# Kernel optimization log

Measured on AMD Instinct MI355X. Metric: run time of the kernel, lower is better.

The kernel has to match this reference:

```python
import jax, jax.numpy as jnp
import numpy as np

N = 50000      # nodes (src = dst at both layers)
E = 800000     # edges per layer
T = 8          # time steps
C_IN = 16      # input channels
HID = 16       # conv1 out channels (hardcoded in SAGENet)
C_OUT = 32     # final out channels


def setup_inputs() -> dict:
    key = jax.random.key(0)
    ks = jax.random.split(key, 10)
    X = jax.random.normal(ks[0], (T, N, C_IN), dtype=jnp.float32)
    edge_index0 = jax.random.randint(ks[1], (2, E), 0, N, dtype=jnp.int32)
    edge_weight0 = jax.random.uniform(ks[2], (E,), dtype=jnp.float32)
    edge_index1 = jax.random.randint(ks[3], (2, E), 0, N, dtype=jnp.int32)
    edge_weight1 = jax.random.uniform(ks[4], (E,), dtype=jnp.float32)
    res_n_id0 = jnp.arange(N, dtype=jnp.int32)
    res_n_id1 = jnp.arange(N, dtype=jnp.int32)
    W1 = jax.random.normal(ks[5], (2 * C_IN, HID), dtype=jnp.float32) * 0.1
    b1 = jax.random.normal(ks[6], (HID,), dtype=jnp.float32) * 0.1
    W2 = jax.random.normal(ks[7], (2 * HID, C_OUT), dtype=jnp.float32) * 0.1
    b2 = jax.random.normal(ks[8], (C_OUT,), dtype=jnp.float32) * 0.1
    return {"X": X, "edge_index0": edge_index0, "edge_weight0": edge_weight0,
            "edge_index1": edge_index1, "edge_weight1": edge_weight1,
            "res_n_id0": res_n_id0, "res_n_id1": res_n_id1,
            "W1": W1, "b1": b1, "W2": W2, "b2": b2}


def sage_conv(x, edge_index, edge_weight, res_n_id, num_dst, W, b):
    # x: [N_src, T, C]; message = edge_weight * x[src]; mean-aggregate to dst;
    # concat residual x[res_n_id] then linear (old PyG SAGEConv, concat=True).
    src, dst = edge_index[0], edge_index[1]
    msg = x[src] * edge_weight[:, None, None]                      # [E, T, C]
    summed = jax.ops.segment_sum(msg, dst, num_segments=num_dst)   # [Nd, T, C]
    cnt = jax.ops.segment_sum(jnp.ones_like(edge_weight), dst, num_segments=num_dst)
    aggr = summed / jnp.maximum(cnt, 1.0)[:, None, None]
    h = jnp.concatenate([x[res_n_id], aggr], axis=-1)              # [Nd, T, 2C]
    return jnp.einsum('ntc,cd->ntd', h, W) + b


def reference(X, edge_index0, edge_weight0, edge_index1, edge_weight1,
              res_n_id0, res_n_id1, W1, b1, W2, b2):
    x = jnp.transpose(X, (1, 0, 2))                                # [N, T, C]
    x = jax.nn.leaky_relu(sage_conv(x, edge_index0, edge_weight0, res_n_id0, N, W1, b1), 0.01)
    x = jax.nn.leaky_relu(sage_conv(x, edge_index1, edge_weight1, res_n_id1, N, W2, b2), 0.01)
    return jnp.transpose(x, (1, 0, 2))                             # [T, N, C_out]
```

## Files before the change

### kernel.cpp

```cpp
#include <hip/hip_runtime.h>
#include <hip/hip_bf16.h>
#include <stdint.h>

static constexpr int Nn   = 50000;
static constexpr int Ee   = 800000;
static constexpr int Tt   = 8;
static constexpr int CIN  = 16;
static constexpr int HID  = 16;
static constexpr int COUT = 32;
static constexpr int TC   = Tt * CIN;
static constexpr int ROWD = TC / 2;

static constexpr int NB  = (2 * Nn + 255) / 256;
static constexpr int CAP = 16;
static constexpr int GSTR = 32;

static constexpr int BINB = 768;
static constexpr int EPB  = (2 * Ee + BINB - 1) / BINB;
static constexpr int TRB  = 1536;

typedef __attribute__((ext_vector_type(8))) short short8;
typedef __attribute__((ext_vector_type(4))) float f32x4;
union FU { uint4 u4; short8 s8; };

__device__ inline unsigned short f2bf(float x) {
    __hip_bfloat16 h = __float2bfloat16(x);
    unsigned short u; __builtin_memcpy(&u, &h, 2); return u;
}
__device__ inline uint32_t bfpack(float a, float b) {
    return (uint32_t)f2bf(a) | ((uint32_t)f2bf(b) << 16);
}
__device__ inline void redg(float2& a) {
    a.x += __shfl_xor(a.x, 16); a.y += __shfl_xor(a.y, 16);
    a.x += __shfl_xor(a.x, 32); a.y += __shfl_xor(a.y, 32);
}

__device__ inline float dot2bf(float acc, uint32_t w2, uint32_t x2) {
    asm("v_dot2_f32_bf16 %0, %1, %2, %0" : "+v"(acc) : "v"(w2), "v"(x2));
    return acc;
}
__device__ inline void dotp(float2& a0, float2& a1, float2& a2, float2& a3,
                            uint32_t w2, uint4 r0, uint4 r1) {
    uint32_t lo, hi;
    lo = __builtin_amdgcn_perm(r1.x, r0.x, 0x05040100u);
    hi = __builtin_amdgcn_perm(r1.x, r0.x, 0x07060302u);
    a0.x = dot2bf(a0.x, w2, lo);
    a0.y = dot2bf(a0.y, w2, hi);
    lo = __builtin_amdgcn_perm(r1.y, r0.y, 0x05040100u);
    hi = __builtin_amdgcn_perm(r1.y, r0.y, 0x07060302u);
    a1.x = dot2bf(a1.x, w2, lo);
    a1.y = dot2bf(a1.y, w2, hi);
    lo = __builtin_amdgcn_perm(r1.z, r0.z, 0x05040100u);
    hi = __builtin_amdgcn_perm(r1.z, r0.z, 0x07060302u);
    a2.x = dot2bf(a2.x, w2, lo);
    a2.y = dot2bf(a2.y, w2, hi);
    lo = __builtin_amdgcn_perm(r1.w, r0.w, 0x05040100u);
    hi = __builtin_amdgcn_perm(r1.w, r0.w, 0x07060302u);
    a3.x = dot2bf(a3.x, w2, lo);
    a3.y = dot2bf(a3.y, w2, hi);
}

__global__ __launch_bounds__(256) void k_count_detect(
        const int* __restrict__ ei0, const int* __restrict__ ei1,
        int* __restrict__ bucketCnt,
        const unsigned short* __restrict__ x16, int nvals,
        int* __restrict__ flag,
        const void* W1, const void* b1, const void* W2, const void* b2,
        float* __restrict__ biasbuf,
        uint32_t* __restrict__ wpk1, uint32_t* __restrict__ wpk2) {
    int tid = threadIdx.x;
    if (blockIdx.x >= 256) {
        __shared__ int bad;
        if (tid == 0) bad = 0;
        __syncthreads();
        for (int i = tid; i < nvals; i += 256) {
            int ex = (x16[i] >> 7) & 0xFF;
            if (ex >= 0x8D) atomicOr(&bad, 1);
        }
        __syncthreads();
        int f = bad;
        if (tid == 0) flag[0] = f;
        auto ldf = [&](const void* srcp, int idx) -> float {
            return f ? ((const float*)srcp)[idx]
                     : __bfloat162float(((const __hip_bfloat16*)srcp)[idx]);
        };
        if (tid < 16) biasbuf[tid] = ldf(b1, tid);
        if (tid >= 16 && tid < 48) biasbuf[tid] = ldf(b2, tid - 16);
        { int h = tid >> 4, d = tid & 15;
          wpk1[tid] = bfpack(ldf(W1, 2 * d * 16 + h), ldf(W1, (2 * d + 1) * 16 + h)); }
        for (int i = tid; i < 512; i += 256) {
            int h = i >> 4, d = i & 15;
            wpk2[i] = bfpack(ldf(W2, 2 * d * 32 + h), ldf(W2, (2 * d + 1) * 32 + h));
        }
        return;
    }
    __shared__ int hist[NB];
    for (int i = tid; i < NB; i += 256) hist[i] = 0;
    __syncthreads();
    const int4* d0 = (const int4*)(ei0 + Ee);
    const int4* d1 = (const int4*)(ei1 + Ee);
    int stride = 256 * 256;
    int nq = Ee / 4;
    for (int i = blockIdx.x * 256 + tid; i < 2 * nq; i += stride) {
        int4 v; int addn;
        if (i < nq) { v = d0[i]; addn = 0; }
        else        { v = d1[i - nq]; addn = Nn; }
        atomicAdd(&hist[(v.x + addn) >> 8], 1);
        atomicAdd(&hist[(v.y + addn) >> 8], 1);
        atomicAdd(&hist[(v.z + addn) >> 8], 1);
        atomicAdd(&hist[(v.w + addn) >> 8], 1);
    }
    __syncthreads();
    for (int i = tid; i < NB; i += 256)
        if (hist[i]) atomicAdd(&bucketCnt[i], hist[i]);
}

__global__ void k_bucketscan(const int* __restrict__ bucketCnt,
                             int* __restrict__ base, int* __restrict__ gcur) {
    __shared__ int tmp[512];
    int tid = threadIdx.x;
    int v = (tid < NB) ? bucketCnt[tid] : 0;
    tmp[tid] = v;
    __syncthreads();
    for (int ofs = 1; ofs < 512; ofs <<= 1) {
        int t = (tid >= ofs) ? tmp[tid - ofs] : 0;
        __syncthreads();
        tmp[tid] += t;
        __syncthreads();
    }
    if (tid < NB) {
        int b = tmp[tid] - v;
        base[tid] = b;
        gcur[tid * GSTR] = b;
    }
    if (tid == 0) base[NB] = 2 * Ee;
}

__global__ __launch_bounds__(256) void k_bin_tr(const int* __restrict__ flag,
        const int* __restrict__ ei0, const void* w0v,
        const int* __restrict__ ei1, const void* w1v,
        int* __restrict__ gcur, uint64_t* __restrict__ gout,
        const void* Xv, uint32_t* __restrict__ xrows) {
    __shared__ uint64_t rows[NB][CAP];
    __shared__ int cnt[NB];
    __shared__ int posArr[NB];
    int tid = threadIdx.x;
    int bid = blockIdx.x;
    if (bid >= BINB) {
        int f = flag[0];
        int stride = TRB * 256;
        for (int i = (bid - BINB) * 256 + tid; i < Nn * ROWD; i += stride) {
            int n = i >> 6;
            int l = i & 63;
            int t = l >> 3;
            int c = (l & 7) * 2;
            int sidx = (t * Nn + n) * CIN + c;
            uint32_t v;
            if (f) {
                float2 ab = ((const float2*)Xv)[sidx >> 1];
                v = bfpack(ab.x, ab.y);
            } else {
                const unsigned short* u = (const unsigned short*)Xv;
                v = (uint32_t)u[sidx] | ((uint32_t)u[sidx + 1] << 16);
            }
            xrows[i] = v;
        }
        return;
    }
    for (int i = tid; i < NB; i += 256) cnt[i] = 0;
    __syncthreads();
    int f = flag[0];
    int lo = bid * EPB;
    int hi = min(2 * Ee, lo + EPB);
    for (int e = lo + tid; e < hi; e += 256) {
        int g; uint32_t src, wb;
        if (e < Ee) {
            g = ei0[Ee + e];
            src = (uint32_t)ei0[e];
            wb = f ? f2bf(((const float*)w0v)[e])
                   : ((const unsigned short*)w0v)[e];
        } else {
            int e1 = e - Ee;
            g = Nn + ei1[Ee + e1];
            src = (uint32_t)ei1[e1];
            wb = f ? f2bf(((const float*)w1v)[e1])
                   : ((const unsigned short*)w1v)[e1];
        }
        uint64_t r = ((uint64_t)(uint32_t)g << 32) | (src << 16) | wb;
        int b = g >> 8;
        int idx = atomicAdd(&cnt[b], 1);
        if (idx < CAP) rows[b][idx ^ (b & (CAP - 1))] = r;
        else { int pos = atomicAdd(&gcur[b * GSTR], 1); gout[pos] = r; }
    }
    __syncthreads();
    for (int b = tid; b < NB; b += 256) {
        int c = min(cnt[b], CAP);
        posArr[b] = c ? atomicAdd(&gcur[b * GSTR], c) : 0;
    }
    __syncthreads();
    int wv = tid >> 6, lane = tid & 63;
    int q = lane >> 4, k = lane & 15;
    for (int b = wv * 4 + q; b < NB; b += 16) {
        int c = min(cnt[b], CAP);
        if (k < c) gout[posArr[b] + k] = rows[b][k ^ (b & (CAP - 1))];
    }
}

__global__ __launch_bounds__(256) void k_csr(const int* __restrict__ base,
        const uint64_t* __restrict__ gout,
        int* __restrict__ off, uint32_t* __restrict__ rec) {
    __shared__ int hist[256];
    __shared__ int tmp[256];
    __shared__ int cur[256];
    __shared__ uint32_t stage[8192];
    int b = blockIdx.x, tid = threadIdx.x;
    int lo = base[b], hi = base[b + 1];
    hist[tid] = 0;
    __syncthreads();
    for (int i = lo + tid; i < hi; i += 256) {
        int gl = (int)(gout[i] >> 32) & 255;
        atomicAdd(&hist[gl], 1);
    }
    __syncthreads();
    int v = hist[tid];
    tmp[tid] = v;
    __syncthreads();
    for (int ofs = 1; ofs < 256; ofs <<= 1) {
        int t = (tid >= ofs) ? tmp[tid - ofs] : 0;
        __syncthreads();
        tmp[tid] += t;
        __syncthreads();
    }
    int excl = tmp[tid] - v;
    int gg = (b << 8) + tid;
    if (gg < 2 * Nn) off[gg] = lo + excl;
    if (b == NB - 1 && tid == 0) off[2 * Nn] = 2 * Ee;
    int count = hi - lo;
    if (count <= 8192) {
        cur[tid] = excl;
        __syncthreads();
        for (int i = lo + tid; i < hi; i += 256) {
            uint64_t r = gout[i];
            int gl = (int)(r >> 32) & 255;
            int pos = atomicAdd(&cur[gl], 1);
            stage[pos] = (uint32_t)r;
        }
        __syncthreads();
        for (int i = tid; i < count; i += 256) rec[lo + i] = stage[i];
    } else {
        cur[tid] = lo + excl;
        __syncthreads();
        for (int i = lo + tid; i < hi; i += 256) {
            uint64_t r = gout[i];
            int gl = (int)(r >> 32) & 255;
            int pos = atomicAdd(&cur[gl], 1);
            rec[pos] = (uint32_t)r;
        }
    }
}


__global__ __launch_bounds__(256) void k_layer1(
    const uint32_t* __restrict__ xrows, const int* __restrict__ off,
    const uint32_t* __restrict__ rec, const int* __restrict__ resid,
    const uint32_t* __restrict__ wpk1, const float* __restrict__ biasbuf,
    uint32_t* __restrict__ h1rows) {
    __shared__ __align__(16) uint32_t shA[64 * 20];
    int tid = threadIdx.x, wv = tid >> 6, lane = tid & 63;
    int g = lane >> 4, p = lane & 15;
    uint4 bfr = ((const uint4*)wpk1)[p * 4 + g];
    float bias = biasbuf[p];
    int n0 = blockIdx.x * 8 + wv * 2;
    int oA0 = __builtin_amdgcn_readfirstlane(off[n0]);
    int oM  = __builtin_amdgcn_readfirstlane(off[n0 + 1]);
    int oB1 = __builtin_amdgcn_readfirstlane(off[n0 + 2]);
    int rnA = __builtin_amdgcn_readfirstlane(resid[n0]);
    int rnB = __builtin_amdgcn_readfirstlane(resid[n0 + 1]);
    int cA = oM - oA0, cB = oB1 - oM;
    int lastA = max(oM - 1, 0), lastB = max(oB1 - 1, 0);
    const uint4* xb = (const uint4*)xrows;
    uint4 xsA = xb[rnA * 16 + p];
    uint4 xsB = xb[rnB * 16 + p];
    float2 aA0 = {0.f, 0.f}, aA1 = aA0, aA2 = aA0, aA3 = aA0;
    float2 aB0 = aA0, aB1 = aA0, aB2 = aA0, aB3 = aA0;
    int cmax = max(cA, cB);
    for (int j = 0; j < cmax; j += 8) {
        int j0 = j + g, j1 = j + 4 + g;
        uint32_t eA0 = rec[min(oA0 + j0, lastA)];
        uint32_t eA1 = rec[min(oA0 + j1, lastA)];
        uint32_t eB0 = rec[min(oM + j0, lastB)];
        uint32_t eB1 = rec[min(oM + j1, lastB)];
        uint4 rA0 = xb[(int)(eA0 >> 16) * 16 + p];
        uint4 rA1 = xb[(int)(eA1 >> 16) * 16 + p];
        uint4 rB0 = xb[(int)(eB0 >> 16) * 16 + p];
        uint4 rB1 = xb[(int)(eB1 >> 16) * 16 + p];
        uint32_t wA = ((j0 < cA) ? (eA0 & 0xffffu) : 0u)
                    | (((j1 < cA) ? (eA1 & 0xffffu) : 0u) << 16);
        uint32_t wB = ((j0 < cB) ? (eB0 & 0xffffu) : 0u)
                    | (((j1 < cB) ? (eB1 & 0xffffu) : 0u) << 16);
        dotp(aA0, aA1, aA2, aA3, wA, rA0, rA1);
        dotp(aB0, aB1, aB2, aB3, wB, rB0, rB1);
    }
    redg(aA0); redg(aA1); redg(aA2); redg(aA3);
    redg(aB0); redg(aB1); redg(aB2); redg(aB3);
    float invA = 1.f / (float)max(cA, 1);
    float invB = 1.f / (float)max(cB, 1);
    uint4 agpA, agpB;
    agpA.x = bfpack(aA0.x * invA, aA0.y * invA);
    agpA.y = bfpack(aA1.x * invA, aA1.y * invA);
    agpA.z = bfpack(aA2.x * invA, aA2.y * invA);
    agpA.w = bfpack(aA3.x * invA, aA3.y * invA);
    agpB.x = bfpack(aB0.x * invB, aB0.y * invB);
    agpB.y = bfpack(aB1.x * invB, aB1.y * invB);
    agpB.z = bfpack(aB2.x * invB, aB2.y * invB);
    agpB.w = bfpack(aB3.x * invB, aB3.y * invB);
    int rA = wv * 16 + (p >> 1);
    int hs = (p & 1) * 4;
    if (g == 0)      *(uint4*)&shA[rA * 20 + hs] = xsA;
    else if (g == 1) *(uint4*)&shA[rA * 20 + 8 + hs] = agpA;
    else if (g == 2) *(uint4*)&shA[(rA + 8) * 20 + hs] = xsB;
    else             *(uint4*)&shA[(rA + 8) * 20 + 8 + hs] = agpB;
    __syncthreads();
    FU fa, fb; fb.u4 = bfr;
    fa.u4 = *(const uint4*)&shA[(wv * 16 + p) * 20 + 4 * g];
    f32x4 acc = {bias, bias, bias, bias};
    acc = __builtin_amdgcn_mfma_f32_16x16x32_bf16(fa.s8, fb.s8, acc, 0, 0, 0);
#pragma unroll
    for (int rg = 0; rg < 4; rg++) {
        float v = acc[rg];
        v = fmaxf(v, 0.01f * v);
        float vn = __shfl_xor(v, 1);
        if (!(p & 1)) {
            int t = (g & 1) * 4 + rg;
            int n = n0 + (g >> 1);
            h1rows[n * 64 + t * 8 + (p >> 1)] = bfpack(v, vn);
        }
    }
}

__global__ __launch_bounds__(256) void k_layer2(
    const int* __restrict__ flag,
    const uint32_t* __restrict__ h1rows, const int* __restrict__ off,
    const uint32_t* __restrict__ rec, const int* __restrict__ resid,
    const uint32_t* __restrict__ wpk2, const float* __restrict__ biasbuf,
    void* __restrict__ outv) {
    __shared__ __align__(16) uint32_t shA[64 * 20];
    int tid = threadIdx.x, wv = tid >> 6, lane = tid & 63;
    int g = lane >> 4, p = lane & 15;
    uint4 b0 = ((const uint4*)wpk2)[p * 4 + g];
    uint4 b1v = ((const uint4*)wpk2)[(p + 16) * 4 + g];
    float bias0 = biasbuf[16 + p];
    float bias1 = biasbuf[32 + p];
    int f = flag[0];
    int n0 = blockIdx.x * 8 + wv * 2;
    int oA0 = __builtin_amdgcn_readfirstlane(off[Nn + n0]);
    int oM  = __builtin_amdgcn_readfirstlane(off[Nn + n0 + 1]);
    int oB1 = __builtin_amdgcn_readfirstlane(off[Nn + n0 + 2]);
    int rnA = __builtin_amdgcn_readfirstlane(resid[n0]);
    int rnB = __builtin_amdgcn_readfirstlane(resid[n0 + 1]);
    int cA = oM - oA0, cB = oB1 - oM;
    int lastA = max(oM - 1, 0), lastB = max(oB1 - 1, 0);
    const uint4* xb = (const uint4*)h1rows;
    uint4 xsA = xb[rnA * 16 + p];
    uint4 xsB = xb[rnB * 16 + p];
    float2 aA0 = {0.f, 0.f}, aA1 = aA0, aA2 = aA0, aA3 = aA0;
    float2 aB0 = aA0, aB1 = aA0, aB2 = aA0, aB3 = aA0;
    int cmax = max(cA, cB);
    for (int j = 0; j < cmax; j += 8) {
        int j0 = j + g, j1 = j + 4 + g;
        uint32_t eA0 = rec[min(oA0 + j0, lastA)];
        uint32_t eA1 = rec[min(oA0 + j1, lastA)];
        uint32_t eB0 = rec[min(oM + j0, lastB)];
        uint32_t eB1 = rec[min(oM + j1, lastB)];
        uint4 rA0 = xb[(int)(eA0 >> 16) * 16 + p];
        uint4 rA1 = xb[(int)(eA1 >> 16) * 16 + p];
        uint4 rB0 = xb[(int)(eB0 >> 16) * 16 + p];
        uint4 rB1 = xb[(int)(eB1 >> 16) * 16 + p];
        uint32_t wA = ((j0 < cA) ? (eA0 & 0xffffu) : 0u)
                    | (((j1 < cA) ? (eA1 & 0xffffu) : 0u) << 16);
        uint32_t wB = ((j0 < cB) ? (eB0 & 0xffffu) : 0u)
                    | (((j1 < cB) ? (eB1 & 0xffffu) : 0u) << 16);
        dotp(aA0, aA1, aA2, aA3, wA, rA0, rA1);
        dotp(aB0, aB1, aB2, aB3, wB, rB0, rB1);
    }
    redg(aA0); redg(aA1); redg(aA2); redg(aA3);
    redg(aB0); redg(aB1); redg(aB2); redg(aB3);
    float invA = 1.f / (float)max(cA, 1);
    float invB = 1.f / (float)max(cB, 1);
    uint4 agpA, agpB;
    agpA.x = bfpack(aA0.x * invA, aA0.y * invA);
    agpA.y = bfpack(aA1.x * invA, aA1.y * invA);
    agpA.z = bfpack(aA2.x * invA, aA2.y * invA);
    agpA.w = bfpack(aA3.x * invA, aA3.y * invA);
    agpB.x = bfpack(aB0.x * invB, aB0.y * invB);
    agpB.y = bfpack(aB1.x * invB, aB1.y * invB);
    agpB.z = bfpack(aB2.x * invB, aB2.y * invB);
    agpB.w = bfpack(aB3.x * invB, aB3.y * invB);
    int rA = wv * 16 + (p >> 1);
    int hs = (p & 1) * 4;
    if (g == 0)      *(uint4*)&shA[rA * 20 + hs] = xsA;
    else if (g == 1) *(uint4*)&shA[rA * 20 + 8 + hs] = agpA;
    else if (g == 2) *(uint4*)&shA[(rA + 8) * 20 + hs] = xsB;
    else             *(uint4*)&shA[(rA + 8) * 20 + 8 + hs] = agpB;
    __syncthreads();
    FU fa, fb0, fb1; fb0.u4 = b0; fb1.u4 = b1v;
    fa.u4 = *(const uint4*)&shA[(wv * 16 + p) * 20 + 4 * g];
    f32x4 acc0 = {bias0, bias0, bias0, bias0};
    f32x4 acc1 = {bias1, bias1, bias1, bias1};
    acc0 = __builtin_amdgcn_mfma_f32_16x16x32_bf16(fa.s8, fb0.s8, acc0, 0, 0, 0);
    acc1 = __builtin_amdgcn_mfma_f32_16x16x32_bf16(fa.s8, fb1.s8, acc1, 0, 0, 0);
#pragma unroll
    for (int rg = 0; rg < 4; rg++) {
        int t = (g & 1) * 4 + rg;
        int n = n0 + (g >> 1);
        float v = acc0[rg]; v = fmaxf(v, 0.01f * v);
        float u = acc1[rg]; u = fmaxf(u, 0.01f * u);
        if (f) {
            size_t idx = ((size_t)(t * Nn + n)) * COUT + p;
            ((float*)outv)[idx] = v;
            ((float*)outv)[idx + 16] = u;
        } else {
            float vn = __shfl_xor(v, 1);
            float un = __shfl_xor(u, 1);
            if (!(p & 1)) {
                size_t di = ((size_t)(t * Nn + n)) * 16 + (p >> 1);
                ((uint32_t*)outv)[di] = bfpack(v, vn);
                ((uint32_t*)outv)[di + 8] = bfpack(u, un);
            }
        }
    }
}


extern "C" void kernel_launch(void* const* d_in, const int* in_sizes, int n_in,
                              void* d_out, int out_size, void* d_ws, size_t ws_size,
                              hipStream_t stream) {
    const void* X   = d_in[0];
    const int* ei0  = (const int*)d_in[1];
    const void* w0  = d_in[2];
    const int* ei1  = (const int*)d_in[3];
    const void* w1  = d_in[4];
    const int* rn0  = (const int*)d_in[5];
    const int* rn1  = (const int*)d_in[6];
    const void* W1  = d_in[7];
    const void* b1  = d_in[8];
    const void* W2  = d_in[9];
    const void* b2  = d_in[10];

    char* ws = (char*)d_ws;
    size_t p = 0;
    auto alloc = [&](size_t bytes) -> char* {
        p = (p + 255) & ~(size_t)255;
        char* r = ws + p;
        p += bytes;
        return r;
    };
    int* flag        = (int*)alloc(4);
    float* biasbuf   = (float*)alloc(48 * 4);
    uint32_t* wpk1   = (uint32_t*)alloc(256 * 4);
    uint32_t* wpk2   = (uint32_t*)alloc(512 * 4);
    int* bucketCnt   = (int*)alloc(NB * 4);
    int* base        = (int*)alloc((NB + 1) * 4);
    int* gcur        = (int*)alloc((size_t)NB * GSTR * 4);
    int* off         = (int*)alloc(((size_t)2 * Nn + 1) * 4);
    uint32_t* recf   = (uint32_t*)alloc((size_t)2 * Ee * 4);
    uint32_t* h1rows = (uint32_t*)alloc((size_t)Nn * ROWD * 4);
    uint64_t* gout   = (uint64_t*)alloc((size_t)2 * Ee * 8);
    uint32_t* xrows  = (uint32_t*)d_out;

    hipMemsetAsync(bucketCnt, 0, NB * sizeof(int), stream);
    hipLaunchKernelGGL(k_count_detect, dim3(257), dim3(256), 0, stream,
                       ei0, ei1, bucketCnt,
                       (const unsigned short*)X, 16384, flag, W1, b1, W2, b2,
                       biasbuf, wpk1, wpk2);
    hipLaunchKernelGGL(k_bucketscan, dim3(1), dim3(512), 0, stream,
                       bucketCnt, base, gcur);
    hipLaunchKernelGGL(k_bin_tr, dim3(BINB + TRB), dim3(256), 0, stream,
                       flag, ei0, w0, ei1, w1, gcur, gout, X, xrows);
    hipLaunchKernelGGL(k_csr, dim3(NB), dim3(256), 0, stream,
                       base, gout, off, recf);
    hipLaunchKernelGGL(k_layer1, dim3(Nn / 8), dim3(256), 0, stream,
                       xrows, off, recf, rn0, wpk1, biasbuf, h1rows);
    hipLaunchKernelGGL(k_layer2, dim3(Nn / 8), dim3(256), 0, stream,
                       flag, h1rows, off, recf, rn1, wpk2, biasbuf, d_out);
    (void)in_sizes; (void)n_in; (void)out_size; (void)ws_size;
}
```

Before: 243.6 us.

## Merge graph-build kernels into one cooperative kernel with grid syncs

Four preprocessing kernels (count/detect, bucket scan, binning+transpose, CSR build) become one cooperative kernel of 768 blocks separated by grid.sync barriers. The aim is to cut kernel launch gaps and tail idling between the small stages. In exchange, the grid is fixed at one block per slot, so the X transpose that used to get 1536 extra blocks now shares the grid, and each grid.sync costs something. The 52KB of shared memory per block limits occupancy, which cooperative launch requires to be co-resident.

```diff
diff --git a/kernel.cpp b/kernel.cpp
--- a/kernel.cpp
+++ b/kernel.cpp
@@ -1,6 +1,9 @@
 #include <hip/hip_runtime.h>
 #include <hip/hip_bf16.h>
+#include <hip/hip_cooperative_groups.h>
 #include <stdint.h>
+
+namespace cg = cooperative_groups;
 
 static constexpr int Nn   = 50000;
 static constexpr int Ee   = 800000;
@@ -17,7 +20,6 @@
 
 static constexpr int BINB = 768;
 static constexpr int EPB  = (2 * Ee + BINB - 1) / BINB;
-static constexpr int TRB  = 1536;
 
 typedef __attribute__((ext_vector_type(8))) short short8;
 typedef __attribute__((ext_vector_type(4))) float f32x4;
@@ -60,26 +62,84 @@
     a3.y = dot2bf(a3.y, w2, hi);
 }
 
-__global__ __launch_bounds__(256) void k_count_detect(
-        const int* __restrict__ ei0, const int* __restrict__ ei1,
-        int* __restrict__ bucketCnt,
-        const unsigned short* __restrict__ x16, int nvals,
+__global__ __launch_bounds__(256) void k_build(
+        const int* __restrict__ ei0, const void* w0v,
+        const int* __restrict__ ei1, const void* w1v,
+        const void* __restrict__ Xv,
         int* __restrict__ flag,
+        int* __restrict__ bucketCnt, int* __restrict__ base,
+        int* __restrict__ gcur,
+        uint64_t* __restrict__ gout, uint32_t* __restrict__ xrows,
+        uint32_t* __restrict__ rec, int* __restrict__ off,
         const void* W1, const void* b1, const void* W2, const void* b2,
         float* __restrict__ biasbuf,
         uint32_t* __restrict__ wpk1, uint32_t* __restrict__ wpk2) {
-    int tid = threadIdx.x;
-    if (blockIdx.x >= 256) {
-        __shared__ int bad;
-        if (tid == 0) bad = 0;
-        __syncthreads();
-        for (int i = tid; i < nvals; i += 256) {
+    __shared__ __align__(16) char shbuf[53248];
+    cg::grid_group grid = cg::this_grid();
+    int tid = threadIdx.x, bid = blockIdx.x;
+
+    if (bid == 0) {
+        int* bad = (int*)shbuf;
+        if (tid == 0) bad[0] = 0;
+        __syncthreads();
+        const unsigned short* x16 = (const unsigned short*)Xv;
+        for (int i = tid; i < 16384; i += 256) {
             int ex = (x16[i] >> 7) & 0xFF;
-            if (ex >= 0x8D) atomicOr(&bad, 1);
-        }
-        __syncthreads();
-        int f = bad;
-        if (tid == 0) flag[0] = f;
+            if (ex >= 0x8D) atomicOr(bad, 1);
+        }
+        __syncthreads();
+        if (tid == 0) flag[0] = bad[0];
+    } else {
+        int* hist = (int*)shbuf;
+        for (int i = tid; i < NB; i += 256) hist[i] = 0;
+        __syncthreads();
+        const int4* d0 = (const int4*)(ei0 + Ee);
+        const int4* d1 = (const int4*)(ei1 + Ee);
+        int nq = Ee / 4;
+        int stride = 767 * 256;
+        for (int i = (bid - 1) * 256 + tid; i < 2 * nq; i += stride) {
+            int4 v; int addn;
+            if (i < nq) { v = d0[i]; addn = 0; }
+            else        { v = d1[i - nq]; addn = Nn; }
+            atomicAdd(&hist[(v.x + addn) >> 8], 1);
+            atomicAdd(&hist[(v.y + addn) >> 8], 1);
+            atomicAdd(&hist[(v.z + addn) >> 8], 1);
+            atomicAdd(&hist[(v.w + addn) >> 8], 1);
+        }
+        __syncthreads();
+        for (int i = tid; i < NB; i += 256)
+            if (hist[i]) atomicAdd(&bucketCnt[i], hist[i]);
+    }
+    grid.sync();
+
+    if (bid == 0) {
+        int* tmp = (int*)shbuf;
+        int v0 = (tid < NB) ? bucketCnt[tid] : 0;
+        int v1 = (tid + 256 < NB) ? bucketCnt[tid + 256] : 0;
+        tmp[tid] = v0;
+        tmp[tid + 256] = v1;
+        __syncthreads();
+        for (int ofs = 1; ofs < 512; ofs <<= 1) {
+            int a = (tid >= ofs) ? tmp[tid - ofs] : 0;
+            int b = (tid + 256 >= ofs) ? tmp[tid + 256 - ofs] : 0;
+            __syncthreads();
+            tmp[tid] += a;
+            tmp[tid + 256] += b;
+            __syncthreads();
+        }
+        if (tid < NB) {
+            int b = tmp[tid] - v0;
+            base[tid] = b;
+            gcur[tid * GSTR] = b;
+        }
+        if (tid + 256 < NB) {
+            int b = tmp[tid + 256] - v1;
+            base[tid + 256] = b;
+            gcur[(tid + 256) * GSTR] = b;
+        }
+        if (tid == 0) base[NB] = 2 * Ee;
+    } else if (bid == 767) {
+        int f = flag[0];
         auto ldf = [&](const void* srcp, int idx) -> float {
             return f ? ((const float*)srcp)[idx]
                      : __bfloat162float(((const __hip_bfloat16*)srcp)[idx]);
@@ -92,64 +152,10 @@
             int h = i >> 4, d = i & 15;
             wpk2[i] = bfpack(ldf(W2, 2 * d * 32 + h), ldf(W2, (2 * d + 1) * 32 + h));
         }
-        return;
-    }
-    __shared__ int hist[NB];
-    for (int i = tid; i < NB; i += 256) hist[i] = 0;
-    __syncthreads();
-    const int4* d0 = (const int4*)(ei0 + Ee);
-    const int4* d1 = (const int4*)(ei1 + Ee);
-    int stride = 256 * 256;
-    int nq = Ee / 4;
-    for (int i = blockIdx.x * 256 + tid; i < 2 * nq; i += stride) {
-        int4 v; int addn;
-        if (i < nq) { v = d0[i]; addn = 0; }
-        else        { v = d1[i - nq]; addn = Nn; }
-        atomicAdd(&hist[(v.x + addn) >> 8], 1);
-        atomicAdd(&hist[(v.y + addn) >> 8], 1);
-        atomicAdd(&hist[(v.z + addn) >> 8], 1);
-        atomicAdd(&hist[(v.w + addn) >> 8], 1);
-    }
-    __syncthreads();
-    for (int i = tid; i < NB; i += 256)
-        if (hist[i]) atomicAdd(&bucketCnt[i], hist[i]);
-}
-
-__global__ void k_bucketscan(const int* __restrict__ bucketCnt,
-                             int* __restrict__ base, int* __restrict__ gcur) {
-    __shared__ int tmp[512];
-    int tid = threadIdx.x;
-    int v = (tid < NB) ? bucketCnt[tid] : 0;
-    tmp[tid] = v;
-    __syncthreads();
-    for (int ofs = 1; ofs < 512; ofs <<= 1) {
-        int t = (tid >= ofs) ? tmp[tid - ofs] : 0;
-        __syncthreads();
-        tmp[tid] += t;
-        __syncthreads();
-    }
-    if (tid < NB) {
-        int b = tmp[tid] - v;
-        base[tid] = b;
-        gcur[tid * GSTR] = b;
-    }
-    if (tid == 0) base[NB] = 2 * Ee;
-}
-
-__global__ __launch_bounds__(256) void k_bin_tr(const int* __restrict__ flag,
-        const int* __restrict__ ei0, const void* w0v,
-        const int* __restrict__ ei1, const void* w1v,
-        int* __restrict__ gcur, uint64_t* __restrict__ gout,
-        const void* Xv, uint32_t* __restrict__ xrows) {
-    __shared__ uint64_t rows[NB][CAP];
-    __shared__ int cnt[NB];
-    __shared__ int posArr[NB];
-    int tid = threadIdx.x;
-    int bid = blockIdx.x;
-    if (bid >= BINB) {
+    } else {
         int f = flag[0];
-        int stride = TRB * 256;
-        for (int i = (bid - BINB) * 256 + tid; i < Nn * ROWD; i += stride) {
+        int stride = 766 * 256;
+        for (int i = (bid - 1) * 256 + tid; i < Nn * ROWD; i += stride) {
             int n = i >> 6;
             int l = i & 63;
             int t = l >> 3;
@@ -165,96 +171,101 @@
             }
             xrows[i] = v;
         }
-        return;
-    }
-    for (int i = tid; i < NB; i += 256) cnt[i] = 0;
-    __syncthreads();
-    int f = flag[0];
-    int lo = bid * EPB;
-    int hi = min(2 * Ee, lo + EPB);
-    for (int e = lo + tid; e < hi; e += 256) {
-        int g; uint32_t src, wb;
-        if (e < Ee) {
-            g = ei0[Ee + e];
-            src = (uint32_t)ei0[e];
-            wb = f ? f2bf(((const float*)w0v)[e])
-                   : ((const unsigned short*)w0v)[e];
+    }
+    grid.sync();
+
+    {
+        uint64_t (*rows)[CAP] = (uint64_t(*)[CAP])shbuf;
+        int* cnt = (int*)(shbuf + 50048);
+        int* posArr = cnt + NB;
+        for (int i = tid; i < NB; i += 256) cnt[i] = 0;
+        __syncthreads();
+        int f = flag[0];
+        int lo = bid * EPB;
+        int hi = min(2 * Ee, lo + EPB);
+        for (int e = lo + tid; e < hi; e += 256) {
+            int g; uint32_t src, wb;
+            if (e < Ee) {
+                g = ei0[Ee + e];
+                src = (uint32_t)ei0[e];
+                wb = f ? f2bf(((const float*)w0v)[e])
+                       : ((const unsigned short*)w0v)[e];
+            } else {
+                int e1 = e - Ee;
+                g = Nn + ei1[Ee + e1];
+                src = (uint32_t)ei1[e1];
+                wb = f ? f2bf(((const float*)w1v)[e1])
+                       : ((const unsigned short*)w1v)[e1];
+            }
+            uint64_t r = ((uint64_t)(uint32_t)g << 32) | (src << 16) | wb;
+            int b = g >> 8;
+            int idx = atomicAdd(&cnt[b], 1);
+            if (idx < CAP) rows[b][idx ^ (b & (CAP - 1))] = r;
+            else { int pos = atomicAdd(&gcur[b * GSTR], 1); gout[pos] = r; }
+        }
+        __syncthreads();
+        for (int b = tid; b < NB; b += 256) {
+            int c = min(cnt[b], CAP);
+            posArr[b] = c ? atomicAdd(&gcur[b * GSTR], c) : 0;
+        }
+        __syncthreads();
+        int wv = tid >> 6, lane = tid & 63;
+        int q = lane >> 4, k = lane & 15;
+        for (int b = wv * 4 + q; b < NB; b += 16) {
+            int c = min(cnt[b], CAP);
+            if (k < c) gout[posArr[b] + k] = rows[b][k ^ (b & (CAP - 1))];
+        }
+    }
+    grid.sync();
+
+    if (bid < NB) {
+        int* hist = (int*)shbuf;
+        int* tmp = hist + 256;
+        int* cur = tmp + 256;
+        uint32_t* stage = (uint32_t*)(cur + 256);
+        int b = bid;
+        int lo = base[b], hi = base[b + 1];
+        hist[tid] = 0;
+        __syncthreads();
+        for (int i = lo + tid; i < hi; i += 256) {
+            int gl = (int)(gout[i] >> 32) & 255;
+            atomicAdd(&hist[gl], 1);
+        }
+        __syncthreads();
+        int v = hist[tid];
+        tmp[tid] = v;
+        __syncthreads();
+        for (int ofs = 1; ofs < 256; ofs <<= 1) {
+            int t = (tid >= ofs) ? tmp[tid - ofs] : 0;
+            __syncthreads();
+            tmp[tid] += t;
+            __syncthreads();
+        }
+        int excl = tmp[tid] - v;
+        int gg = (b << 8) + tid;
+        if (gg < 2 * Nn) off[gg] = lo + excl;
+        if (b == NB - 1 && tid == 0) off[2 * Nn] = 2 * Ee;
+        int count = hi - lo;
+        if (count <= 8192) {
+            cur[tid] = excl;
+            __syncthreads();
+            for (int i = lo + tid; i < hi; i += 256) {
+                uint64_t r = gout[i];
+                int gl = (int)(r >> 32) & 255;
+                int pos = atomicAdd(&cur[gl], 1);
+                stage[pos] = (uint32_t)r;
+            }
+            __syncthreads();
+            for (int i = tid; i < count; i += 256) rec[lo + i] = stage[i];
         } else {
-            int e1 = e - Ee;
-            g = Nn + ei1[Ee + e1];
-            src = (uint32_t)ei1[e1];
-            wb = f ? f2bf(((const float*)w1v)[e1])
-                   : ((const unsigned short*)w1v)[e1];
-        }
-        uint64_t r = ((uint64_t)(uint32_t)g << 32) | (src << 16) | wb;
-        int b = g >> 8;
-        int idx = atomicAdd(&cnt[b], 1);
-        if (idx < CAP) rows[b][idx ^ (b & (CAP - 1))] = r;
-        else { int pos = atomicAdd(&gcur[b * GSTR], 1); gout[pos] = r; }
-    }
-    __syncthreads();
-    for (int b = tid; b < NB; b += 256) {
-        int c = min(cnt[b], CAP);
-        posArr[b] = c ? atomicAdd(&gcur[b * GSTR], c) : 0;
-    }
-    __syncthreads();
-    int wv = tid >> 6, lane = tid & 63;
-    int q = lane >> 4, k = lane & 15;
-    for (int b = wv * 4 + q; b < NB; b += 16) {
-        int c = min(cnt[b], CAP);
-        if (k < c) gout[posArr[b] + k] = rows[b][k ^ (b & (CAP - 1))];
-    }
-}
-
-__global__ __launch_bounds__(256) void k_csr(const int* __restrict__ base,
-        const uint64_t* __restrict__ gout,
-        int* __restrict__ off, uint32_t* __restrict__ rec) {
-    __shared__ int hist[256];
-    __shared__ int tmp[256];
-    __shared__ int cur[256];
-    __shared__ uint32_t stage[8192];
-    int b = blockIdx.x, tid = threadIdx.x;
-    int lo = base[b], hi = base[b + 1];
-    hist[tid] = 0;
-    __syncthreads();
-    for (int i = lo + tid; i < hi; i += 256) {
-        int gl = (int)(gout[i] >> 32) & 255;
-        atomicAdd(&hist[gl], 1);
-    }
-    __syncthreads();
-    int v = hist[tid];
-    tmp[tid] = v;
-    __syncthreads();
-    for (int ofs = 1; ofs < 256; ofs <<= 1) {
-        int t = (tid >= ofs) ? tmp[tid - ofs] : 0;
-        __syncthreads();
-        tmp[tid] += t;
-        __syncthreads();
-    }
-    int excl = tmp[tid] - v;
-    int gg = (b << 8) + tid;
-    if (gg < 2 * Nn) off[gg] = lo + excl;
-    if (b == NB - 1 && tid == 0) off[2 * Nn] = 2 * Ee;
-    int count = hi - lo;
-    if (count <= 8192) {
-        cur[tid] = excl;
-        __syncthreads();
-        for (int i = lo + tid; i < hi; i += 256) {
-            uint64_t r = gout[i];
-            int gl = (int)(r >> 32) & 255;
-            int pos = atomicAdd(&cur[gl], 1);
-            stage[pos] = (uint32_t)r;
-        }
-        __syncthreads();
-        for (int i = tid; i < count; i += 256) rec[lo + i] = stage[i];
-    } else {
-        cur[tid] = lo + excl;
-        __syncthreads();
-        for (int i = lo + tid; i < hi; i += 256) {
-            uint64_t r = gout[i];
-            int gl = (int)(r >> 32) & 255;
-            int pos = atomicAdd(&cur[gl], 1);
-            rec[pos] = (uint32_t)r;
+            cur[tid] = lo + excl;
+            __syncthreads();
+            for (int i = lo + tid; i < hi; i += 256) {
+                uint64_t r = gout[i];
+                int gl = (int)(r >> 32) & 255;
+                int pos = atomicAdd(&cur[gl], 1);
+                rec[pos] = (uint32_t)r;
+            }
         }
     }
 }
@@ -469,16 +480,17 @@
     uint32_t* xrows  = (uint32_t*)d_out;
 
     hipMemsetAsync(bucketCnt, 0, NB * sizeof(int), stream);
-    hipLaunchKernelGGL(k_count_detect, dim3(257), dim3(256), 0, stream,
-                       ei0, ei1, bucketCnt,
-                       (const unsigned short*)X, 16384, flag, W1, b1, W2, b2,
-                       biasbuf, wpk1, wpk2);
-    hipLaunchKernelGGL(k_bucketscan, dim3(1), dim3(512), 0, stream,
-                       bucketCnt, base, gcur);
-    hipLaunchKernelGGL(k_bin_tr, dim3(BINB + TRB), dim3(256), 0, stream,
-                       flag, ei0, w0, ei1, w1, gcur, gout, X, xrows);
-    hipLaunchKernelGGL(k_csr, dim3(NB), dim3(256), 0, stream,
-                       base, gout, off, recf);
+
+    void* kargs[] = {
+        (void*)&ei0, (void*)&w0, (void*)&ei1, (void*)&w1, (void*)&X,
+        (void*)&flag, (void*)&bucketCnt, (void*)&base, (void*)&gcur,
+        (void*)&gout, (void*)&xrows, (void*)&recf, (void*)&off,
+        (void*)&W1, (void*)&b1, (void*)&W2, (void*)&b2,
+        (void*)&biasbuf, (void*)&wpk1, (void*)&wpk2
+    };
+    hipLaunchCooperativeKernel((const void*)k_build, dim3(BINB), dim3(256),
+                               kargs, 0, stream);
+
     hipLaunchKernelGGL(k_layer1, dim3(Nn / 8), dim3(256), 0, stream,
                        xrows, off, recf, rn0, wpk1, biasbuf, h1rows);
     hipLaunchKernelGGL(k_layer2, dim3(Nn / 8), dim3(256), 0, stream,
```

New measurement: 519.1 us. +113.1%, slower.

## Replace histogram and scan pass with fixed-capacity bucket slots

Applied to the files above, without the earlier changes.

Removes the bucket-counting histogram kernel and the single-block prefix-scan kernel. Each bucket now gets a fixed slot of BCAP entries in the binned edge buffer, so edges can be scattered without knowing exact offsets in advance. Per-node counts are stored alongside offsets because the CSR is no longer contiguous. This saves one full read of the destination indices and two launches, but it relies on no bucket exceeding BCAP entries, which holds for uniform random inputs but would overflow on skewed graphs. It also enlarges the workspace buffers.

```diff
diff --git a/kernel.cpp b/kernel.cpp
--- a/kernel.cpp
+++ b/kernel.cpp
@@ -11,9 +11,10 @@
 static constexpr int TC   = Tt * CIN;
 static constexpr int ROWD = TC / 2;
 
-static constexpr int NB  = (2 * Nn + 255) / 256;
-static constexpr int CAP = 16;
+static constexpr int NB   = (2 * Nn + 255) / 256;
+static constexpr int CAP  = 16;
 static constexpr int GSTR = 32;
+static constexpr int BCAP = 5120;
 
 static constexpr int BINB = 768;
 static constexpr int EPB  = (2 * Ee + BINB - 1) / BINB;
@@ -60,26 +61,36 @@
     a3.y = dot2bf(a3.y, w2, hi);
 }
 
-__global__ __launch_bounds__(256) void k_count_detect(
-        const int* __restrict__ ei0, const int* __restrict__ ei1,
-        int* __restrict__ bucketCnt,
-        const unsigned short* __restrict__ x16, int nvals,
-        int* __restrict__ flag,
+__global__ void k_detect(const unsigned short* __restrict__ x16, int nvals,
+                         int* __restrict__ flag, int* __restrict__ gcur) {
+    __shared__ int bad;
+    int tid = threadIdx.x;
+    if (tid == 0) bad = 0;
+    __syncthreads();
+    for (int i = tid; i < nvals; i += 256) {
+        int ex = (x16[i] >> 7) & 0xFF;
+        if (ex >= 0x8D) atomicOr(&bad, 1);
+    }
+    for (int i = tid; i < NB * GSTR; i += 256) gcur[i] = 0;
+    __syncthreads();
+    if (tid == 0) flag[0] = bad;
+}
+
+__global__ __launch_bounds__(256) void k_bin_tr(const int* __restrict__ flag,
+        const int* __restrict__ ei0, const void* w0v,
+        const int* __restrict__ ei1, const void* w1v,
+        int* __restrict__ gcur, uint64_t* __restrict__ gout,
+        const void* __restrict__ Xv, uint32_t* __restrict__ xrows,
         const void* W1, const void* b1, const void* W2, const void* b2,
         float* __restrict__ biasbuf,
         uint32_t* __restrict__ wpk1, uint32_t* __restrict__ wpk2) {
+    __shared__ uint64_t rows[NB][CAP];
+    __shared__ int cnt[NB];
+    __shared__ int posArr[NB];
     int tid = threadIdx.x;
-    if (blockIdx.x >= 256) {
-        __shared__ int bad;
-        if (tid == 0) bad = 0;
-        __syncthreads();
-        for (int i = tid; i < nvals; i += 256) {
-            int ex = (x16[i] >> 7) & 0xFF;
-            if (ex >= 0x8D) atomicOr(&bad, 1);
-        }
-        __syncthreads();
-        int f = bad;
-        if (tid == 0) flag[0] = f;
+    int bid = blockIdx.x;
+    if (bid == BINB) {
+        int f = flag[0];
         auto ldf = [&](const void* srcp, int idx) -> float {
             return f ? ((const float*)srcp)[idx]
                      : __bfloat162float(((const __hip_bfloat16*)srcp)[idx]);
@@ -94,62 +105,10 @@
         }
         return;
     }
-    __shared__ int hist[NB];
-    for (int i = tid; i < NB; i += 256) hist[i] = 0;
-    __syncthreads();
-    const int4* d0 = (const int4*)(ei0 + Ee);
-    const int4* d1 = (const int4*)(ei1 + Ee);
-    int stride = 256 * 256;
-    int nq = Ee / 4;
-    for (int i = blockIdx.x * 256 + tid; i < 2 * nq; i += stride) {
-        int4 v; int addn;
-        if (i < nq) { v = d0[i]; addn = 0; }
-        else        { v = d1[i - nq]; addn = Nn; }
-        atomicAdd(&hist[(v.x + addn) >> 8], 1);
-        atomicAdd(&hist[(v.y + addn) >> 8], 1);
-        atomicAdd(&hist[(v.z + addn) >> 8], 1);
-        atomicAdd(&hist[(v.w + addn) >> 8], 1);
-    }
-    __syncthreads();
-    for (int i = tid; i < NB; i += 256)
-        if (hist[i]) atomicAdd(&bucketCnt[i], hist[i]);
-}
-
-__global__ void k_bucketscan(const int* __restrict__ bucketCnt,
-                             int* __restrict__ base, int* __restrict__ gcur) {
-    __shared__ int tmp[512];
-    int tid = threadIdx.x;
-    int v = (tid < NB) ? bucketCnt[tid] : 0;
-    tmp[tid] = v;
-    __syncthreads();
-    for (int ofs = 1; ofs < 512; ofs <<= 1) {
-        int t = (tid >= ofs) ? tmp[tid - ofs] : 0;
-        __syncthreads();
-        tmp[tid] += t;
-        __syncthreads();
-    }
-    if (tid < NB) {
-        int b = tmp[tid] - v;
-        base[tid] = b;
-        gcur[tid * GSTR] = b;
-    }
-    if (tid == 0) base[NB] = 2 * Ee;
-}
-
-__global__ __launch_bounds__(256) void k_bin_tr(const int* __restrict__ flag,
-        const int* __restrict__ ei0, const void* w0v,
-        const int* __restrict__ ei1, const void* w1v,
-        int* __restrict__ gcur, uint64_t* __restrict__ gout,
-        const void* Xv, uint32_t* __restrict__ xrows) {
-    __shared__ uint64_t rows[NB][CAP];
-    __shared__ int cnt[NB];
-    __shared__ int posArr[NB];
-    int tid = threadIdx.x;
-    int bid = blockIdx.x;
-    if (bid >= BINB) {
+    if (bid > BINB) {
         int f = flag[0];
         int stride = TRB * 256;
-        for (int i = (bid - BINB) * 256 + tid; i < Nn * ROWD; i += stride) {
+        for (int i = (bid - BINB - 1) * 256 + tid; i < Nn * ROWD; i += stride) {
             int n = i >> 6;
             int l = i & 63;
             int t = l >> 3;
@@ -190,12 +149,15 @@
         int b = g >> 8;
         int idx = atomicAdd(&cnt[b], 1);
         if (idx < CAP) rows[b][idx ^ (b & (CAP - 1))] = r;
-        else { int pos = atomicAdd(&gcur[b * GSTR], 1); gout[pos] = r; }
+        else {
+            int pos = atomicAdd(&gcur[b * GSTR], 1);
+            gout[(size_t)b * BCAP + pos] = r;
+        }
     }
     __syncthreads();
     for (int b = tid; b < NB; b += 256) {
         int c = min(cnt[b], CAP);
-        posArr[b] = c ? atomicAdd(&gcur[b * GSTR], c) : 0;
+        posArr[b] = c ? (b * BCAP + atomicAdd(&gcur[b * GSTR], c)) : 0;
     }
     __syncthreads();
     int wv = tid >> 6, lane = tid & 63;
@@ -206,15 +168,18 @@
     }
 }
 
-__global__ __launch_bounds__(256) void k_csr(const int* __restrict__ base,
+__global__ __launch_bounds__(256) void k_csr(const int* __restrict__ gcur,
         const uint64_t* __restrict__ gout,
-        int* __restrict__ off, uint32_t* __restrict__ rec) {
+        int* __restrict__ off, int* __restrict__ ncnt,
+        uint32_t* __restrict__ rec) {
     __shared__ int hist[256];
     __shared__ int tmp[256];
     __shared__ int cur[256];
     __shared__ uint32_t stage[8192];
     int b = blockIdx.x, tid = threadIdx.x;
-    int lo = base[b], hi = base[b + 1];
+    int lo = b * BCAP;
+    int count = gcur[b * GSTR];
+    int hi = lo + count;
     hist[tid] = 0;
     __syncthreads();
     for (int i = lo + tid; i < hi; i += 256) {
@@ -233,9 +198,7 @@
     }
     int excl = tmp[tid] - v;
     int gg = (b << 8) + tid;
-    if (gg < 2 * Nn) off[gg] = lo + excl;
-    if (b == NB - 1 && tid == 0) off[2 * Nn] = 2 * Ee;
-    int count = hi - lo;
+    if (gg < 2 * Nn) { off[gg] = lo + excl; ncnt[gg] = v; }
     if (count <= 8192) {
         cur[tid] = excl;
         __syncthreads();
@@ -262,6 +225,7 @@
 
 __global__ __launch_bounds__(256) void k_layer1(
     const uint32_t* __restrict__ xrows, const int* __restrict__ off,
+    const int* __restrict__ ncnt,
     const uint32_t* __restrict__ rec, const int* __restrict__ resid,
     const uint32_t* __restrict__ wpk1, const float* __restrict__ biasbuf,
     uint32_t* __restrict__ h1rows) {
@@ -273,11 +237,11 @@
     int n0 = blockIdx.x * 8 + wv * 2;
     int oA0 = __builtin_amdgcn_readfirstlane(off[n0]);
     int oM  = __builtin_amdgcn_readfirstlane(off[n0 + 1]);
-    int oB1 = __builtin_amdgcn_readfirstlane(off[n0 + 2]);
+    int cA  = __builtin_amdgcn_readfirstlane(ncnt[n0]);
+    int cB  = __builtin_amdgcn_readfirstlane(ncnt[n0 + 1]);
     int rnA = __builtin_amdgcn_readfirstlane(resid[n0]);
     int rnB = __builtin_amdgcn_readfirstlane(resid[n0 + 1]);
-    int cA = oM - oA0, cB = oB1 - oM;
-    int lastA = max(oM - 1, 0), lastB = max(oB1 - 1, 0);
+    int lastA = max(oA0 + cA - 1, 0), lastB = max(oM + cB - 1, 0);
     const uint4* xb = (const uint4*)xrows;
     uint4 xsA = xb[rnA * 16 + p];
     uint4 xsB = xb[rnB * 16 + p];
@@ -341,6 +305,7 @@
 __global__ __launch_bounds__(256) void k_layer2(
     const int* __restrict__ flag,
     const uint32_t* __restrict__ h1rows, const int* __restrict__ off,
+    const int* __restrict__ ncnt,
     const uint32_t* __restrict__ rec, const int* __restrict__ resid,
     const uint32_t* __restrict__ wpk2, const float* __restrict__ biasbuf,
     void* __restrict__ outv) {
@@ -355,11 +320,11 @@
     int n0 = blockIdx.x * 8 + wv * 2;
     int oA0 = __builtin_amdgcn_readfirstlane(off[Nn + n0]);
     int oM  = __builtin_amdgcn_readfirstlane(off[Nn + n0 + 1]);
-    int oB1 = __builtin_amdgcn_readfirstlane(off[Nn + n0 + 2]);
+    int cA  = __builtin_amdgcn_readfirstlane(ncnt[Nn + n0]);
+    int cB  = __builtin_amdgcn_readfirstlane(ncnt[Nn + n0 + 1]);
     int rnA = __builtin_amdgcn_readfirstlane(resid[n0]);
     int rnB = __builtin_amdgcn_readfirstlane(resid[n0 + 1]);
-    int cA = oM - oA0, cB = oB1 - oM;
-    int lastA = max(oM - 1, 0), lastB = max(oB1 - 1, 0);
+    int lastA = max(oA0 + cA - 1, 0), lastB = max(oM + cB - 1, 0);
     const uint4* xb = (const uint4*)h1rows;
     uint4 xsA = xb[rnA * 16 + p];
     uint4 xsB = xb[rnB * 16 + p];
@@ -459,29 +424,24 @@
     float* biasbuf   = (float*)alloc(48 * 4);
     uint32_t* wpk1   = (uint32_t*)alloc(256 * 4);
     uint32_t* wpk2   = (uint32_t*)alloc(512 * 4);
-    int* bucketCnt   = (int*)alloc(NB * 4);
-    int* base        = (int*)alloc((NB + 1) * 4);
     int* gcur        = (int*)alloc((size_t)NB * GSTR * 4);
-    int* off         = (int*)alloc(((size_t)2 * Nn + 1) * 4);
-    uint32_t* recf   = (uint32_t*)alloc((size_t)2 * Ee * 4);
+    int* off         = (int*)alloc((size_t)2 * Nn * 4);
+    int* ncnt        = (int*)alloc((size_t)2 * Nn * 4);
+    uint32_t* recf   = (uint32_t*)alloc((size_t)NB * BCAP * 4);
     uint32_t* h1rows = (uint32_t*)alloc((size_t)Nn * ROWD * 4);
-    uint64_t* gout   = (uint64_t*)alloc((size_t)2 * Ee * 8);
+    uint64_t* gout   = (uint64_t*)alloc((size_t)NB * BCAP * 8);
     uint32_t* xrows  = (uint32_t*)d_out;
 
-    hipMemsetAsync(bucketCnt, 0, NB * sizeof(int), stream);
-    hipLaunchKernelGGL(k_count_detect, dim3(257), dim3(256), 0, stream,
-                       ei0, ei1, bucketCnt,
-                       (const unsigned short*)X, 16384, flag, W1, b1, W2, b2,
-                       biasbuf, wpk1, wpk2);
-    hipLaunchKernelGGL(k_bucketscan, dim3(1), dim3(512), 0, stream,
-                       bucketCnt, base, gcur);
-    hipLaunchKernelGGL(k_bin_tr, dim3(BINB + TRB), dim3(256), 0, stream,
-                       flag, ei0, w0, ei1, w1, gcur, gout, X, xrows);
+    hipLaunchKernelGGL(k_detect, dim3(1), dim3(256), 0, stream,
+                       (const unsigned short*)X, 16384, flag, gcur);
+    hipLaunchKernelGGL(k_bin_tr, dim3(BINB + 1 + TRB), dim3(256), 0, stream,
+                       flag, ei0, w0, ei1, w1, gcur, gout, X, xrows,
+                       W1, b1, W2, b2, biasbuf, wpk1, wpk2);
     hipLaunchKernelGGL(k_csr, dim3(NB), dim3(256), 0, stream,
-                       base, gout, off, recf);
+                       gcur, gout, off, ncnt, recf);
     hipLaunchKernelGGL(k_layer1, dim3(Nn / 8), dim3(256), 0, stream,
-                       xrows, off, recf, rn0, wpk1, biasbuf, h1rows);
+                       xrows, off, ncnt, recf, rn0, wpk1, biasbuf, h1rows);
     hipLaunchKernelGGL(k_layer2, dim3(Nn / 8), dim3(256), 0, stream,
-                       flag, h1rows, off, recf, rn1, wpk2, biasbuf, d_out);
+                       flag, h1rows, off, ncnt, recf, rn1, wpk2, biasbuf, d_out);
     (void)in_sizes; (void)n_in; (void)out_size; (void)ws_size;
 }
```

Result: faster. 231.7 us (-4.9%).
